# Kernel optimization log

Hardware: AMD Instinct MI355X
Metric: run time of the kernel (lower is better)

The kernel has to match this reference:

```python
import jax, jax.numpy as jnp
import numpy as np


def gcn_conv(x, W, b, src, dst, num_nodes):
    """PyG GCNConv with add_self_loops=True, symmetric normalization, bias.
    src/dst already include self-loops. deg computed from unit edge weights."""
    deg = jax.ops.segment_sum(jnp.ones(src.shape[0], x.dtype), dst,
                              num_segments=num_nodes)
    dinv = jnp.where(deg > 0, jax.lax.rsqrt(deg), 0.0)
    norm = dinv[src] * dinv[dst]               # [E]
    h = x @ W                                  # [N, F_out] dense GEMM first
    msg = h[src] * norm[:, None]               # gather + scale, [E, F_out]
    out = jax.ops.segment_sum(msg, dst, num_segments=num_nodes)  # scatter-add
    return out + b


def setup_inputs() -> dict:
    key = jax.random.key(0)
    ks = jax.random.split(key, 5)
    N, E, F_in, F_out = 50000, 800000, 512, 40
    x = jax.random.normal(ks[0], (N, F_in), dtype=jnp.float32)
    edge_index = jax.random.randint(ks[1], (2, E), 0, N, dtype=jnp.int64)
    W1 = jax.random.normal(ks[2], (F_in, 256), dtype=jnp.float32) * (F_in ** -0.5)
    W2 = jax.random.normal(ks[3], (256, 16), dtype=jnp.float32) * (256 ** -0.5)
    W3 = jax.random.normal(ks[4], (16, F_out), dtype=jnp.float32) * (16 ** -0.5)
    return {
        "x": x, "edge_index": edge_index,
        "W1": W1, "b1": jnp.zeros((256,), jnp.float32),
        "W2": W2, "b2": jnp.zeros((16,), jnp.float32),
        "W3": W3, "b3": jnp.zeros((F_out,), jnp.float32),
    }


def reference(x, edge_index, W1, b1, W2, b2, W3, b3):
    N = x.shape[0]
    loop = jnp.arange(N, dtype=edge_index.dtype)
    src = jnp.concatenate([edge_index[0], loop])  # self-loops appended once,
    dst = jnp.concatenate([edge_index[1], loop])  # shared by all three layers
    h = gcn_conv(x, W1, b1, src, dst, N)
    h = jax.nn.relu(h)                 # dropout is identity in eval mode
    h = gcn_conv(h, W2, b2, src, dst, N)
    h = jax.nn.relu(h)
    h = gcn_conv(h, W3, b3, src, dst, N)
    return jax.nn.log_softmax(h, axis=1)
```

## Files before the change

kernel.cpp:

```cpp
#include <hip/hip_runtime.h>
#include <hip/hip_bf16.h>
#include <math.h>

typedef __hip_bfloat16 bf16;
typedef __attribute__((ext_vector_type(8))) __bf16 bf16x8;
typedef __attribute__((ext_vector_type(4))) float f32x4;

#define KIN 512
#define F1  256
#define F2  16
#define F3  40
#define NBIN 64
#define TSS 264


__device__ inline unsigned pk_bf2(float a, float b) {
  bf16 x = __float2bfloat16(a), y = __float2bfloat16(b);
  unsigned short ux = *(unsigned short*)&x, uy = *(unsigned short*)&y;
  return (unsigned)ux | ((unsigned)uy << 16);
}
__device__ inline float bfbits(unsigned u16) {
  unsigned v = u16 << 16;
  return *(float*)&v;
}
__device__ inline void async16(const void* g, void* l) {
  __builtin_amdgcn_global_load_lds((const __attribute__((address_space(1))) void*)g,
                                   (__attribute__((address_space(3))) void*)l, 16, 0, 0);
}
__device__ inline void accum8(float* acc, uint4 h, float w) {
  acc[0] = fmaf(w, bfbits(h.x & 0xffff), acc[0]);
  acc[1] = fmaf(w, bfbits(h.x >> 16),    acc[1]);
  acc[2] = fmaf(w, bfbits(h.y & 0xffff), acc[2]);
  acc[3] = fmaf(w, bfbits(h.y >> 16),    acc[3]);
  acc[4] = fmaf(w, bfbits(h.z & 0xffff), acc[4]);
  acc[5] = fmaf(w, bfbits(h.z >> 16),    acc[5]);
  acc[6] = fmaf(w, bfbits(h.w & 0xffff), acc[6]);
  acc[7] = fmaf(w, bfbits(h.w >> 16),    acc[7]);
}


__global__ __launch_bounds__(256) void k_init2(int* __restrict__ cnt,
                                               const int* __restrict__ ei, int* __restrict__ flag,
                                               const float* __restrict__ W,
                                               unsigned short* __restrict__ Wt,
                                               int* __restrict__ hist,
                                               int n, int nb) {
  int b = blockIdx.x;
  int t = threadIdx.x;
  if (b < nb) {
    int i = b * 256 + t;
    if (i < n) cnt[i] = 0;
    if (b == 0 && t < NBIN) hist[t] = 0;
    if (b == 0 && t == 0)
      *flag = (ei[1] == 0 && ei[3] == 0 && ei[5] == 0 && ei[7] == 0) ? 1 : 0;
  } else {
    __shared__ float tile[32][33];
    int b2 = b - nb;
    int k0 = (b2 & 15) * 32;
    int n0 = (b2 >> 4) * 32;
    int lr = t >> 5, lc = t & 31;
#pragma unroll
    for (int rr = 0; rr < 32; rr += 8)
      tile[lr + rr][lc] = W[(size_t)(k0 + lr + rr) * F1 + n0 + lc];
    __syncthreads();
#pragma unroll
    for (int rr = 0; rr < 32; rr += 8) {
      bf16 v = __float2bfloat16(tile[lc][lr + rr]);
      Wt[(size_t)(n0 + lr + rr) * KIN + k0 + lc] = *(unsigned short*)&v;
    }
  }
}


__global__ __launch_bounds__(256) void k_count_conv(const int* __restrict__ ei,
                                                    const int* __restrict__ flag,
                                                    int* __restrict__ cnt,
                                                    int* __restrict__ rank,
                                                    int E, int nct, int stride,
                                                    const float* __restrict__ X,
                                                    unsigned short* __restrict__ Xb,
                                                    int total8) {
  int b = blockIdx.x;
  int t = threadIdx.x;
  bool is_cnt = (b % stride == 0) && (b / stride < nct);
  if (is_cnt) {
    int e = (b / stride) * 256 + t;
    if (e >= E) return;
    int is64 = *flag;
    int d = is64 ? ei[2 * E + 2 * e] : ei[E + e];
    rank[e] = atomicAdd(&cnt[d], 1);
  } else {
    int nb_before = (b + stride - 1) / stride;
    if (nb_before > nct) nb_before = nct;
    int idx = (b - nb_before) * 256 + t;
    if (idx >= total8) return;
    const float4* src = (const float4*)X + (size_t)idx * 2;
    float4 f0 = src[0], f1 = src[1];
    uint4 pk;
    pk.x = pk_bf2(f0.x, f0.y); pk.y = pk_bf2(f0.z, f0.w);
    pk.z = pk_bf2(f1.x, f1.y); pk.w = pk_bf2(f1.z, f1.w);
    ((uint4*)Xb)[idx] = pk;
  }
}

__global__ __launch_bounds__(256) void k_scan1(const int* __restrict__ cnt,
                                               int* __restrict__ off,
                                               int* __restrict__ bsum,
                                               float* __restrict__ dinv,
                                               int* __restrict__ hist, int N) {
  __shared__ int s[256];
  __shared__ int lh[NBIN];
  int t = threadIdx.x;
  if (t < NBIN) lh[t] = 0;
  int base = blockIdx.x * 1024 + t * 4;
  int v0 = (base + 0 < N) ? cnt[base + 0] : 0;
  int v1 = (base + 1 < N) ? cnt[base + 1] : 0;
  int v2 = (base + 2 < N) ? cnt[base + 2] : 0;
  int v3 = (base + 3 < N) ? cnt[base + 3] : 0;
  if (base + 0 < N) dinv[base + 0] = rsqrtf((float)(v0 + 1));
  if (base + 1 < N) dinv[base + 1] = rsqrtf((float)(v1 + 1));
  if (base + 2 < N) dinv[base + 2] = rsqrtf((float)(v2 + 1));
  if (base + 3 < N) dinv[base + 3] = rsqrtf((float)(v3 + 1));
  int tsum = v0 + v1 + v2 + v3;
  s[t] = tsum;
  __syncthreads();
  if (base + 0 < N) atomicAdd(&lh[v0 < 63 ? v0 : 63], 1);
  if (base + 1 < N) atomicAdd(&lh[v1 < 63 ? v1 : 63], 1);
  if (base + 2 < N) atomicAdd(&lh[v2 < 63 ? v2 : 63], 1);
  if (base + 3 < N) atomicAdd(&lh[v3 < 63 ? v3 : 63], 1);
  for (int d = 1; d < 256; d <<= 1) {
    int u = (t >= d) ? s[t - d] : 0;
    __syncthreads();
    s[t] += u;
    __syncthreads();
  }
  int excl = s[t] - tsum;
  int p0 = excl + v0, p1 = p0 + v1, p2 = p1 + v2, p3 = p2 + v3;
  if (base + 0 < N) off[base + 1] = p0;
  if (base + 1 < N) off[base + 2] = p1;
  if (base + 2 < N) off[base + 3] = p2;
  if (base + 3 < N) off[base + 4] = p3;
  if (t == 255) bsum[blockIdx.x] = s[255];
  if (t < NBIN) {
    int h = lh[t];
    if (h) atomicAdd(&hist[t], h);
  }
}

__global__ __launch_bounds__(256) void k_scan3m(int* __restrict__ off,
                                                const int* __restrict__ bsum,
                                                const int* __restrict__ hist,
                                                int* __restrict__ binoff, int N) {
  __shared__ int cs;
  int t = threadIdx.x;
  if (t < 64) {
    int v = (t < blockIdx.x) ? bsum[t] : 0;
    for (int d = 32; d; d >>= 1) v += __shfl_xor(v, d, 64);
    if (t == 0) cs = v;
  }
  if (blockIdx.x == 0 && t < NBIN) {
    int a = 0;
    for (int j = t + 1; j < NBIN; ++j) a += hist[j];
    binoff[t] = a;
  }
  __syncthreads();
  int c = cs;
  int base = blockIdx.x * 1024 + t * 4;
#pragma unroll
  for (int k = 0; k < 4; ++k)
    if (base + k < N) off[base + k + 1] += c;
  if (blockIdx.x == 0 && t == 0) off[0] = 0;
}


__global__ __launch_bounds__(256) void k_gemm1_sc(const unsigned short* __restrict__ Ab,
                                                  const unsigned short* __restrict__ Bt,
                                                  bf16* __restrict__ C, int M, int ngx,
                                                  const int* __restrict__ ei,
                                                  const int* __restrict__ flag,
                                                  const int* __restrict__ off,
                                                  const int* __restrict__ rank,
                                                  const float* __restrict__ dinv,
                                                  int2* __restrict__ ew, int E, int ebk,
                                                  const int* __restrict__ cnt,
                                                  int* __restrict__ binoff,
                                                  int* __restrict__ perm) {
  __shared__ unsigned short As[128 * 32];
  __shared__ unsigned short Bs[128 * 32];
  __shared__ int lh[NBIN], lb[NBIN];
  int b = blockIdx.x;
  int t = threadIdx.x;
  int ngemm = ngx * 2;
  if (b >= ngemm + ebk) {
    int idx = (b - ngemm - ebk) * 256 + t;
    if (t < NBIN) lh[t] = 0;
    __syncthreads();
    int bin = 0, lr2 = 0;
    bool valid = (idx < M);
    if (valid) {
      int d = cnt[idx];
      bin = d < 63 ? d : 63;
      lr2 = atomicAdd(&lh[bin], 1);
    }
    __syncthreads();
    if (t < NBIN && lh[t] > 0) lb[t] = atomicAdd(&binoff[t], lh[t]);
    __syncthreads();
    if (valid) perm[lb[bin] + lr2] = idx;
    return;
  }
  if (b >= ngemm) {
    int e = (b - ngemm) * 256 + t;
    if (e >= E) return;
    int is64 = *flag;
    int s, d;
    if (is64) { s = ei[2 * e]; d = ei[2 * E + 2 * e]; }
    else      { s = ei[e];     d = ei[E + e]; }
    int pos = off[d] + rank[e];
    float w = dinv[s] * dinv[d];
    ew[pos] = make_int2(s, __float_as_int(w));
    return;
  }
  int wave = t >> 6, lane = t & 63;
  int wm = wave >> 1, wn = wave & 1;
  int row0 = (b % ngx) * 128, col0 = (b / ngx) * 128;
  int q = lane >> 4, m16 = lane & 15;
  int srow = lane >> 2, schk = lane & 3;

  f32x4 acc[4][4];
#pragma unroll
  for (int i = 0; i < 4; ++i)
#pragma unroll
    for (int j = 0; j < 4; ++j) acc[i][j] = {0.f, 0.f, 0.f, 0.f};

  for (int kb = 0; kb < 16; ++kb) {
    __syncthreads();
#pragma unroll
    for (int jj = 0; jj < 2; ++jj) {
      int lr = wave * 32 + jj * 16 + srow;
      int gr = row0 + lr; if (gr >= M) gr = M - 1;
      int gchk = schk ^ ((lr >> 1) & 3);
      async16(Ab + (size_t)gr * KIN + kb * 32 + gchk * 8,
              As + (wave * 32 + jj * 16) * 32);
    }
#pragma unroll
    for (int jj = 0; jj < 2; ++jj) {
      int lr = wave * 32 + jj * 16 + srow;
      int gchk = schk ^ ((lr >> 1) & 3);
      async16(Bt + (size_t)(col0 + lr) * KIN + kb * 32 + gchk * 8,
              Bs + (wave * 32 + jj * 16) * 32);
    }
    __syncthreads();
    bf16x8 af[4], bfr[4];
#pragma unroll
    for (int i = 0; i < 4; ++i) {
      int m = wm * 64 + i * 16 + m16;
      af[i] = *(const bf16x8*)(As + m * 32 + ((q ^ ((m >> 1) & 3)) * 8));
    }
#pragma unroll
    for (int j = 0; j < 4; ++j) {
      int n = wn * 64 + j * 16 + m16;
      bfr[j] = *(const bf16x8*)(Bs + n * 32 + ((q ^ ((n >> 1) & 3)) * 8));
    }
#pragma unroll
    for (int j = 0; j < 4; ++j)
#pragma unroll
      for (int i = 0; i < 4; ++i)
        acc[i][j] = __builtin_amdgcn_mfma_f32_16x16x32_bf16(af[i], bfr[j], acc[i][j], 0, 0, 0);
  }

#pragma unroll
  for (int i = 0; i < 4; ++i) {
#pragma unroll
    for (int r = 0; r < 4; ++r) {
      int row = row0 + wm * 64 + i * 16 + q * 4 + r;
      if (row < M) {
#pragma unroll
        for (int j = 0; j < 4; ++j) {
          int col = col0 + wn * 64 + j * 16 + m16;
          C[(size_t)row * F1 + col] = __float2bfloat16(acc[i][j][r]);
        }
      }
    }
  }
}


__global__ __launch_bounds__(256) void k_agg1g2(const bf16* __restrict__ H,
                                                const int* __restrict__ off,
                                                const int2* __restrict__ ew,
                                                const float* __restrict__ dinv,
                                                const float* __restrict__ b1,
                                                const int* __restrict__ perm,
                                                const float* __restrict__ W2,
                                                float* __restrict__ h2, int N) {
  __shared__ float W2s[F1 * F2];
  __shared__ float Ts[8][TSS];
  int t = threadIdx.x;
#pragma unroll
  for (int j = 0; j < 16; ++j) W2s[t + 256 * j] = W2[t + 256 * j];
  int idx = blockIdx.x * 8 + (t >> 5);
  int cidx = idx < N ? idx : N - 1;
  int i = perm[cidx];
  int f0 = (t & 31) * 8;
  const unsigned short* Hu = (const unsigned short*)H;
  float di = dinv[i];
  float w0 = di * di;
  float acc[8];
  {
    uint4 h = *(const uint4*)(Hu + (size_t)i * F1 + f0);
    acc[0] = w0 * bfbits(h.x & 0xffff); acc[1] = w0 * bfbits(h.x >> 16);
    acc[2] = w0 * bfbits(h.y & 0xffff); acc[3] = w0 * bfbits(h.y >> 16);
    acc[4] = w0 * bfbits(h.z & 0xffff); acc[5] = w0 * bfbits(h.z >> 16);
    acc[6] = w0 * bfbits(h.w & 0xffff); acc[7] = w0 * bfbits(h.w >> 16);
  }
  int e = off[i], e1 = off[i + 1];
  for (; e + 8 <= e1; e += 8) {
    int2 p0 = ew[e + 0], p1 = ew[e + 1], p2 = ew[e + 2], p3 = ew[e + 3];
    int2 p4 = ew[e + 4], p5 = ew[e + 5], p6 = ew[e + 6], p7 = ew[e + 7];
    uint4 g0 = *(const uint4*)(Hu + (size_t)p0.x * F1 + f0);
    uint4 g1 = *(const uint4*)(Hu + (size_t)p1.x * F1 + f0);
    uint4 g2 = *(const uint4*)(Hu + (size_t)p2.x * F1 + f0);
    uint4 g3 = *(const uint4*)(Hu + (size_t)p3.x * F1 + f0);
    uint4 g4 = *(const uint4*)(Hu + (size_t)p4.x * F1 + f0);
    uint4 g5 = *(const uint4*)(Hu + (size_t)p5.x * F1 + f0);
    uint4 g6 = *(const uint4*)(Hu + (size_t)p6.x * F1 + f0);
    uint4 g7 = *(const uint4*)(Hu + (size_t)p7.x * F1 + f0);
    accum8(acc, g0, __int_as_float(p0.y));
    accum8(acc, g1, __int_as_float(p1.y));
    accum8(acc, g2, __int_as_float(p2.y));
    accum8(acc, g3, __int_as_float(p3.y));
    accum8(acc, g4, __int_as_float(p4.y));
    accum8(acc, g5, __int_as_float(p5.y));
    accum8(acc, g6, __int_as_float(p6.y));
    accum8(acc, g7, __int_as_float(p7.y));
  }
  for (; e < e1; ++e) {
    int2 pe = ew[e];
    uint4 g = *(const uint4*)(Hu + (size_t)pe.x * F1 + f0);
    accum8(acc, g, __int_as_float(pe.y));
  }
  float4 bb0 = *(const float4*)(b1 + f0);
  float4 bb1 = *(const float4*)(b1 + f0 + 4);
  int node = t >> 5;
  float* ts = &Ts[node][f0];
  ts[0] = fmaxf(acc[0] + bb0.x, 0.f);
  ts[1] = fmaxf(acc[1] + bb0.y, 0.f);
  ts[2] = fmaxf(acc[2] + bb0.z, 0.f);
  ts[3] = fmaxf(acc[3] + bb0.w, 0.f);
  ts[4] = fmaxf(acc[4] + bb1.x, 0.f);
  ts[5] = fmaxf(acc[5] + bb1.y, 0.f);
  ts[6] = fmaxf(acc[6] + bb1.z, 0.f);
  ts[7] = fmaxf(acc[7] + bb1.w, 0.f);
  __syncthreads();
  if (t < 128) {
    int n2 = t >> 4, c = t & 15;
    int gi = blockIdx.x * 8 + n2;
    float s = 0.f;
    const float4* tv = (const float4*)&Ts[n2][0];
#pragma unroll 8
    for (int k4 = 0; k4 < 64; ++k4) {
      float4 a = tv[k4];
      int k = k4 * 4;
      s = fmaf(a.x, W2s[(k + 0) * 16 + c], s);
      s = fmaf(a.y, W2s[(k + 1) * 16 + c], s);
      s = fmaf(a.z, W2s[(k + 2) * 16 + c], s);
      s = fmaf(a.w, W2s[(k + 3) * 16 + c], s);
    }
    if (gi < N) h2[(size_t)perm[gi] * F2 + c] = s;
  }
}


__global__ __launch_bounds__(256) void k_agg16(const float* __restrict__ H,
                                               const int* __restrict__ off,
                                               const int2* __restrict__ ew,
                                               const float* __restrict__ dinv,
                                               const float* __restrict__ bias,
                                               const int* __restrict__ perm,
                                               float* __restrict__ O, int N) {
  int t = threadIdx.x;
  int idx = blockIdx.x * 16 + (t >> 4);
  int f = t & 15;
  if (idx >= N) return;
  int i = perm[idx];
  float di = dinv[i];
  float acc = di * di * H[(size_t)i * F2 + f];
  int e = off[i], e1 = off[i + 1];
  for (; e + 4 <= e1; e += 4) {
    int2 p0 = ew[e + 0], p1 = ew[e + 1], p2 = ew[e + 2], p3 = ew[e + 3];
    float g0 = H[(size_t)p0.x * F2 + f];
    float g1 = H[(size_t)p1.x * F2 + f];
    float g2 = H[(size_t)p2.x * F2 + f];
    float g3 = H[(size_t)p3.x * F2 + f];
    acc = fmaf(__int_as_float(p0.y), g0, acc);
    acc = fmaf(__int_as_float(p1.y), g1, acc);
    acc = fmaf(__int_as_float(p2.y), g2, acc);
    acc = fmaf(__int_as_float(p3.y), g3, acc);
  }
  for (; e < e1; ++e) {
    int2 pe = ew[e];
    acc = fmaf(__int_as_float(pe.y), H[(size_t)pe.x * F2 + f], acc);
  }
  acc = fmaxf(acc + bias[f], 0.f);
  O[(size_t)i * F2 + f] = acc;
}


__global__ __launch_bounds__(256) void k_agg3_g3(const float* __restrict__ H,
                                                 const int* __restrict__ off,
                                                 const int2* __restrict__ ew,
                                                 const float* __restrict__ dinv,
                                                 const float* __restrict__ W3,
                                                 const float* __restrict__ b3,
                                                 const int* __restrict__ perm,
                                                 float* __restrict__ O, int N) {
  __shared__ float W3s[F2 * F3];
  __shared__ float b3s[F3];
  __shared__ float aggs[16 * 17];
  int t = threadIdx.x;
  for (int idx2 = t; idx2 < F2 * F3; idx2 += 256) W3s[idx2] = W3[idx2];
  if (t < F3) b3s[t] = b3[t];
  __syncthreads();

  int node = t >> 4, f = t & 15;
  int idx = blockIdx.x * 16 + node;
  if (idx >= N) return;
  int i = perm[idx];
  float di = dinv[i];
  float acc = di * di * H[(size_t)i * F2 + f];
  int e = off[i], e1 = off[i + 1];
  for (; e + 4 <= e1; e += 4) {
    int2 p0 = ew[e + 0], p1 = ew[e + 1], p2 = ew[e + 2], p3 = ew[e + 3];
    float g0 = H[(size_t)p0.x * F2 + f];
    float g1 = H[(size_t)p1.x * F2 + f];
    float g2 = H[(size_t)p2.x * F2 + f];
    float g3 = H[(size_t)p3.x * F2 + f];
    acc = fmaf(__int_as_float(p0.y), g0, acc);
    acc = fmaf(__int_as_float(p1.y), g1, acc);
    acc = fmaf(__int_as_float(p2.y), g2, acc);
    acc = fmaf(__int_as_float(p3.y), g3, acc);
  }
  for (; e < e1; ++e) {
    int2 pe = ew[e];
    acc = fmaf(__int_as_float(pe.y), H[(size_t)pe.x * F2 + f], acc);
  }
  aggs[node * 17 + f] = acc;

  const float* ar = &aggs[node * 17];
  float o0 = b3s[f], o1 = b3s[f + 16], o2 = (f < 8) ? b3s[f + 32] : 0.f;
#pragma unroll
  for (int k = 0; k < F2; ++k) {
    float a = ar[k];
    o0 = fmaf(a, W3s[k * F3 + f], o0);
    o1 = fmaf(a, W3s[k * F3 + f + 16], o1);
    if (f < 8) o2 = fmaf(a, W3s[k * F3 + f + 32], o2);
  }
  float m = fmaxf(o0, o1);
  if (f < 8) m = fmaxf(m, o2);
#pragma unroll
  for (int d = 1; d < 16; d <<= 1) m = fmaxf(m, __shfl_xor(m, d, 16));
  float s = __expf(o0 - m) + __expf(o1 - m) + ((f < 8) ? __expf(o2 - m) : 0.f);
#pragma unroll
  for (int d = 1; d < 16; d <<= 1) s += __shfl_xor(s, d, 16);
  float lse = m + __logf(s);
  float* orow = O + (size_t)i * F3;
  orow[f] = o0 - lse;
  orow[f + 16] = o1 - lse;
  if (f < 8) orow[f + 32] = o2 - lse;
}


extern "C" void kernel_launch(void* const* d_in, const int* in_sizes, int n_in,
                              void* d_out, int out_size, void* d_ws, size_t ws_size,
                              hipStream_t stream) {
  const float* x  = (const float*)d_in[0];
  const int*   ei = (const int*)d_in[1];
  const float* W1 = (const float*)d_in[2];
  const float* b1 = (const float*)d_in[3];
  const float* W2 = (const float*)d_in[4];
  const float* b2 = (const float*)d_in[5];
  const float* W3 = (const float*)d_in[6];
  const float* b3 = (const float*)d_in[7];
  float* out = (float*)d_out;

  int N = in_sizes[0] / KIN;
  int E = in_sizes[1] / 2;

  char* p = (char*)d_ws;
  auto take = [&](size_t bytes) {
    char* r = p;
    p += (bytes + 255) & ~(size_t)255;
    return r;
  };
  int*   flag  = (int*)take(4);
  int*   cnt   = (int*)take((size_t)N * 4);
  int*   off   = (int*)take((size_t)(N + 1) * 4);
  float* dinv  = (float*)take((size_t)N * 4);
  int*   bsum  = (int*)take(64 * 4);
  int*   hist  = (int*)take(NBIN * 4);
  int*   binoff= (int*)take(NBIN * 4);
  int*   perm  = (int*)take((size_t)N * 4);
  int*   rank  = (int*)take((size_t)E * 4);
  int2*  ew    = (int2*)take((size_t)E * 8);
  unsigned short* w1t = (unsigned short*)take((size_t)KIN * F1 * 2);
  unsigned short* xb  = (unsigned short*)take((size_t)N * KIN * 2);
  bf16*  h1    = (bf16*)take((size_t)N * F1 * 2);
  float* h2    = (float*)take((size_t)N * F2 * 4);
  float* out2  = (float*)take((size_t)N * F2 * 4);

  int nb  = (N + 255) / 256;
  int ebk = (E + 255) / 256;
  int nsc = (N + 1023) / 1024;
  int total8 = (N * KIN) / 8;
  int cvb = (total8 + 255) / 256;
  int tot = ebk + cvb;
  int stride = tot / ebk; if (stride < 1) stride = 1;

  k_init2<<<nb + 128, 256, 0, stream>>>(cnt, ei, flag, W1, w1t, hist, N, nb);
  k_count_conv<<<tot, 256, 0, stream>>>(ei, flag, cnt, rank, E, ebk, stride, x, xb, total8);
  k_scan1<<<nsc, 256, 0, stream>>>(cnt, off, bsum, dinv, hist, N);
  k_scan3m<<<nsc, 256, 0, stream>>>(off, bsum, hist, binoff, N);

  int ngx = (N + 127) / 128;
  k_gemm1_sc<<<ngx * 2 + ebk + nb, 256, 0, stream>>>(xb, w1t, h1, N, ngx,
                                                     ei, flag, off, rank, dinv, ew, E, ebk,
                                                     cnt, binoff, perm);

  k_agg1g2<<<(N + 7) / 8, 256, 0, stream>>>(h1, off, ew, dinv, b1, perm, W2, h2, N);
  k_agg16<<<(N + 15) / 16, 256, 0, stream>>>(h2, off, ew, dinv, b2, perm, out2, N);
  k_agg3_g3<<<(N + 15) / 16, 256, 0, stream>>>(out2, off, ew, dinv, W3, b3, perm, out, N);
}
```

Measured before the change: 322.7 us.

## Fuse fp32-to-bf16 conversion into GEMM A-load and register-shuffle the W2 projection

The separate pass that converted x to a bf16 buffer is removed. The GEMM now reads fp32 rows of x directly, packs them to bf16 in registers and stores them into the swizzled LDS tile, which avoids writing and re-reading a 51 MB intermediate. Because the grid has two column blocks, each x tile is read in fp32 twice, and those loads are now synchronous instead of async-to-LDS. Separately, the layer-1 aggregation kernel drops its shared-memory staging of W2 and the activations. It computes the 256x16 projection with per-lane partial products and a butterfly shuffle reduction, trading LDS and a barrier for more registers and global W2 reads.

```diff
diff --git a/kernel.cpp b/kernel.cpp
--- a/kernel.cpp
+++ b/kernel.cpp
@@ -11,7 +11,6 @@
 #define F2  16
 #define F3  40
 #define NBIN 64
-#define TSS 264
 
 
 __device__ inline unsigned pk_bf2(float a, float b) {
@@ -72,35 +71,15 @@
 }
 
 
-__global__ __launch_bounds__(256) void k_count_conv(const int* __restrict__ ei,
-                                                    const int* __restrict__ flag,
-                                                    int* __restrict__ cnt,
-                                                    int* __restrict__ rank,
-                                                    int E, int nct, int stride,
-                                                    const float* __restrict__ X,
-                                                    unsigned short* __restrict__ Xb,
-                                                    int total8) {
-  int b = blockIdx.x;
-  int t = threadIdx.x;
-  bool is_cnt = (b % stride == 0) && (b / stride < nct);
-  if (is_cnt) {
-    int e = (b / stride) * 256 + t;
-    if (e >= E) return;
-    int is64 = *flag;
-    int d = is64 ? ei[2 * E + 2 * e] : ei[E + e];
-    rank[e] = atomicAdd(&cnt[d], 1);
-  } else {
-    int nb_before = (b + stride - 1) / stride;
-    if (nb_before > nct) nb_before = nct;
-    int idx = (b - nb_before) * 256 + t;
-    if (idx >= total8) return;
-    const float4* src = (const float4*)X + (size_t)idx * 2;
-    float4 f0 = src[0], f1 = src[1];
-    uint4 pk;
-    pk.x = pk_bf2(f0.x, f0.y); pk.y = pk_bf2(f0.z, f0.w);
-    pk.z = pk_bf2(f1.x, f1.y); pk.w = pk_bf2(f1.z, f1.w);
-    ((uint4*)Xb)[idx] = pk;
-  }
+__global__ __launch_bounds__(256) void k_count(const int* __restrict__ ei,
+                                               const int* __restrict__ flag,
+                                               int* __restrict__ cnt,
+                                               int* __restrict__ rank, int E) {
+  int e = blockIdx.x * 256 + threadIdx.x;
+  if (e >= E) return;
+  int is64 = *flag;
+  int d = is64 ? ei[2 * E + 2 * e] : ei[E + e];
+  rank[e] = atomicAdd(&cnt[d], 1);
 }
 
 __global__ __launch_bounds__(256) void k_scan1(const int* __restrict__ cnt,
@@ -173,7 +152,7 @@
 }
 
 
-__global__ __launch_bounds__(256) void k_gemm1_sc(const unsigned short* __restrict__ Ab,
+__global__ __launch_bounds__(256) void k_gemm1_sc(const float* __restrict__ X,
                                                   const unsigned short* __restrict__ Bt,
                                                   bf16* __restrict__ C, int M, int ngx,
                                                   const int* __restrict__ ei,
@@ -185,8 +164,8 @@
                                                   const int* __restrict__ cnt,
                                                   int* __restrict__ binoff,
                                                   int* __restrict__ perm) {
-  __shared__ unsigned short As[128 * 32];
-  __shared__ unsigned short Bs[128 * 32];
+  __shared__ __align__(16) unsigned short As[128 * 32];
+  __shared__ __align__(16) unsigned short Bs[128 * 32];
   __shared__ int lh[NBIN], lb[NBIN];
   int b = blockIdx.x;
   int t = threadIdx.x;
@@ -226,6 +205,15 @@
   int q = lane >> 4, m16 = lane & 15;
   int srow = lane >> 2, schk = lane & 3;
 
+  int ar = t >> 1;
+  int as0 = (t & 1) * 2;
+  int agr = row0 + ar; if (agr >= M) agr = M - 1;
+  int ag0 = as0 ^ ((ar >> 1) & 3);
+  int ag1 = (as0 + 1) ^ ((ar >> 1) & 3);
+  const float* xrow = X + (size_t)agr * KIN;
+  uint4* aslot0 = (uint4*)(As + ar * 32 + as0 * 8);
+  uint4* aslot1 = (uint4*)(As + ar * 32 + (as0 + 1) * 8);
+
   f32x4 acc[4][4];
 #pragma unroll
   for (int i = 0; i < 4; ++i)
@@ -234,14 +222,10 @@
 
   for (int kb = 0; kb < 16; ++kb) {
     __syncthreads();
-#pragma unroll
-    for (int jj = 0; jj < 2; ++jj) {
-      int lr = wave * 32 + jj * 16 + srow;
-      int gr = row0 + lr; if (gr >= M) gr = M - 1;
-      int gchk = schk ^ ((lr >> 1) & 3);
-      async16(Ab + (size_t)gr * KIN + kb * 32 + gchk * 8,
-              As + (wave * 32 + jj * 16) * 32);
-    }
+    const float4* pa0 = (const float4*)(xrow + kb * 32 + ag0 * 8);
+    const float4* pa1 = (const float4*)(xrow + kb * 32 + ag1 * 8);
+    float4 a00 = pa0[0], a01 = pa0[1];
+    float4 a10 = pa1[0], a11 = pa1[1];
 #pragma unroll
     for (int jj = 0; jj < 2; ++jj) {
       int lr = wave * 32 + jj * 16 + srow;
@@ -249,6 +233,13 @@
       async16(Bt + (size_t)(col0 + lr) * KIN + kb * 32 + gchk * 8,
               Bs + (wave * 32 + jj * 16) * 32);
     }
+    uint4 w0, w1;
+    w0.x = pk_bf2(a00.x, a00.y); w0.y = pk_bf2(a00.z, a00.w);
+    w0.z = pk_bf2(a01.x, a01.y); w0.w = pk_bf2(a01.z, a01.w);
+    w1.x = pk_bf2(a10.x, a10.y); w1.y = pk_bf2(a10.z, a10.w);
+    w1.z = pk_bf2(a11.x, a11.y); w1.w = pk_bf2(a11.z, a11.w);
+    *aslot0 = w0;
+    *aslot1 = w1;
     __syncthreads();
     bf16x8 af[4], bfr[4];
 #pragma unroll
@@ -293,15 +284,12 @@
                                                 const int* __restrict__ perm,
                                                 const float* __restrict__ W2,
                                                 float* __restrict__ h2, int N) {
-  __shared__ float W2s[F1 * F2];
-  __shared__ float Ts[8][TSS];
-  int t = threadIdx.x;
-#pragma unroll
-  for (int j = 0; j < 16; ++j) W2s[t + 256 * j] = W2[t + 256 * j];
+  int t = threadIdx.x;
   int idx = blockIdx.x * 8 + (t >> 5);
   int cidx = idx < N ? idx : N - 1;
   int i = perm[cidx];
-  int f0 = (t & 31) * 8;
+  int gl = t & 31;
+  int f0 = gl * 8;
   const unsigned short* Hu = (const unsigned short*)H;
   float di = dinv[i];
   float w0 = di * di;
@@ -341,33 +329,55 @@
   }
   float4 bb0 = *(const float4*)(b1 + f0);
   float4 bb1 = *(const float4*)(b1 + f0 + 4);
-  int node = t >> 5;
-  float* ts = &Ts[node][f0];
-  ts[0] = fmaxf(acc[0] + bb0.x, 0.f);
-  ts[1] = fmaxf(acc[1] + bb0.y, 0.f);
-  ts[2] = fmaxf(acc[2] + bb0.z, 0.f);
-  ts[3] = fmaxf(acc[3] + bb0.w, 0.f);
-  ts[4] = fmaxf(acc[4] + bb1.x, 0.f);
-  ts[5] = fmaxf(acc[5] + bb1.y, 0.f);
-  ts[6] = fmaxf(acc[6] + bb1.z, 0.f);
-  ts[7] = fmaxf(acc[7] + bb1.w, 0.f);
-  __syncthreads();
-  if (t < 128) {
-    int n2 = t >> 4, c = t & 15;
-    int gi = blockIdx.x * 8 + n2;
-    float s = 0.f;
-    const float4* tv = (const float4*)&Ts[n2][0];
-#pragma unroll 8
-    for (int k4 = 0; k4 < 64; ++k4) {
-      float4 a = tv[k4];
-      int k = k4 * 4;
-      s = fmaf(a.x, W2s[(k + 0) * 16 + c], s);
-      s = fmaf(a.y, W2s[(k + 1) * 16 + c], s);
-      s = fmaf(a.z, W2s[(k + 2) * 16 + c], s);
-      s = fmaf(a.w, W2s[(k + 3) * 16 + c], s);
-    }
-    if (gi < N) h2[(size_t)perm[gi] * F2 + c] = s;
-  }
+  float r8[8];
+  r8[0] = fmaxf(acc[0] + bb0.x, 0.f); r8[1] = fmaxf(acc[1] + bb0.y, 0.f);
+  r8[2] = fmaxf(acc[2] + bb0.z, 0.f); r8[3] = fmaxf(acc[3] + bb0.w, 0.f);
+  r8[4] = fmaxf(acc[4] + bb1.x, 0.f); r8[5] = fmaxf(acc[5] + bb1.y, 0.f);
+  r8[6] = fmaxf(acc[6] + bb1.z, 0.f); r8[7] = fmaxf(acc[7] + bb1.w, 0.f);
+  float p[16];
+#pragma unroll
+  for (int c = 0; c < 16; ++c) p[c] = 0.f;
+#pragma unroll
+  for (int f = 0; f < 8; ++f) {
+    float rv = r8[f];
+    const float4* wr = (const float4*)(W2 + (size_t)(f0 + f) * 16);
+    float4 w0v = wr[0], w1v = wr[1], w2v = wr[2], w3v = wr[3];
+    p[0]  = fmaf(rv, w0v.x, p[0]);  p[1]  = fmaf(rv, w0v.y, p[1]);
+    p[2]  = fmaf(rv, w0v.z, p[2]);  p[3]  = fmaf(rv, w0v.w, p[3]);
+    p[4]  = fmaf(rv, w1v.x, p[4]);  p[5]  = fmaf(rv, w1v.y, p[5]);
+    p[6]  = fmaf(rv, w1v.z, p[6]);  p[7]  = fmaf(rv, w1v.w, p[7]);
+    p[8]  = fmaf(rv, w2v.x, p[8]);  p[9]  = fmaf(rv, w2v.y, p[9]);
+    p[10] = fmaf(rv, w2v.z, p[10]); p[11] = fmaf(rv, w2v.w, p[11]);
+    p[12] = fmaf(rv, w3v.x, p[12]); p[13] = fmaf(rv, w3v.y, p[13]);
+    p[14] = fmaf(rv, w3v.z, p[14]); p[15] = fmaf(rv, w3v.w, p[15]);
+  }
+#pragma unroll
+  for (int c = 0; c < 16; ++c) p[c] += __shfl_xor(p[c], 16, 32);
+#pragma unroll
+  for (int c = 0; c < 8; ++c) {
+    float keep = (gl & 8) ? p[c + 8] : p[c];
+    float send = (gl & 8) ? p[c] : p[c + 8];
+    p[c] = keep + __shfl_xor(send, 8, 32);
+  }
+#pragma unroll
+  for (int c = 0; c < 4; ++c) {
+    float keep = (gl & 4) ? p[c + 4] : p[c];
+    float send = (gl & 4) ? p[c] : p[c + 4];
+    p[c] = keep + __shfl_xor(send, 4, 32);
+  }
+#pragma unroll
+  for (int c = 0; c < 2; ++c) {
+    float keep = (gl & 2) ? p[c + 2] : p[c];
+    float send = (gl & 2) ? p[c] : p[c + 2];
+    p[c] = keep + __shfl_xor(send, 2, 32);
+  }
+  {
+    float keep = (gl & 1) ? p[1] : p[0];
+    float send = (gl & 1) ? p[0] : p[1];
+    p[0] = keep + __shfl_xor(send, 1, 32);
+  }
+  if ((gl & 16) == 0 && idx < N)
+    h2[(size_t)i * F2 + gl] = p[0];
 }
 
 
@@ -503,7 +513,6 @@
   int*   rank  = (int*)take((size_t)E * 4);
   int2*  ew    = (int2*)take((size_t)E * 8);
   unsigned short* w1t = (unsigned short*)take((size_t)KIN * F1 * 2);
-  unsigned short* xb  = (unsigned short*)take((size_t)N * KIN * 2);
   bf16*  h1    = (bf16*)take((size_t)N * F1 * 2);
   float* h2    = (float*)take((size_t)N * F2 * 4);
   float* out2  = (float*)take((size_t)N * F2 * 4);
@@ -511,18 +520,14 @@
   int nb  = (N + 255) / 256;
   int ebk = (E + 255) / 256;
   int nsc = (N + 1023) / 1024;
-  int total8 = (N * KIN) / 8;
-  int cvb = (total8 + 255) / 256;
-  int tot = ebk + cvb;
-  int stride = tot / ebk; if (stride < 1) stride = 1;
 
   k_init2<<<nb + 128, 256, 0, stream>>>(cnt, ei, flag, W1, w1t, hist, N, nb);
-  k_count_conv<<<tot, 256, 0, stream>>>(ei, flag, cnt, rank, E, ebk, stride, x, xb, total8);
+  k_count<<<ebk, 256, 0, stream>>>(ei, flag, cnt, rank, E);
   k_scan1<<<nsc, 256, 0, stream>>>(cnt, off, bsum, dinv, hist, N);
   k_scan3m<<<nsc, 256, 0, stream>>>(off, bsum, hist, binoff, N);
 
   int ngx = (N + 127) / 128;
-  k_gemm1_sc<<<ngx * 2 + ebk + nb, 256, 0, stream>>>(xb, w1t, h1, N, ngx,
+  k_gemm1_sc<<<ngx * 2 + ebk + nb, 256, 0, stream>>>(x, w1t, h1, N, ngx,
                                                      ei, flag, off, rank, dinv, ew, E, ebk,
                                                      cnt, binoff, perm);
 
```

Result: slower. 415.4 us (+28.7%).
